# Kernel tuning notes

Measured on AMD Instinct MI355X. Metric: run time of the kernel, lower is better.

Reference implementation:

```python
import jax, jax.numpy as jnp
import numpy as np

EPS = 1e-3  # tfa LayerNormLSTMCell default norm epsilon

def _ln(z, g, b):
    # layernorm over last axis, per gate: z [B,4,U], g/b [4,U]
    mu = jnp.mean(z, axis=-1, keepdims=True)
    var = jnp.mean((z - mu) ** 2, axis=-1, keepdims=True)
    return g * (z - mu) * jax.lax.rsqrt(var + EPS) + b

def setup_inputs() -> dict:
    key = jax.random.key(0)
    ks = jax.random.split(key, 12)
    B, T, D, U, C = 1024, 100, 300, 512, 14
    sc = lambda k, shape, fan: jax.random.normal(k, shape, jnp.float32) * (1.0 / np.sqrt(fan))
    return {
        "x": jax.random.normal(ks[0], (B, T, D), jnp.float32),
        "mask": jax.random.randint(ks[1], (B, T), 0, 2).astype(jnp.int32),
        # layer 0 (input dim D)
        "W0": sc(ks[2], (D, 4 * U), D), "U0": sc(ks[3], (U, 4 * U), U),
        "b0": jnp.zeros((4 * U,), jnp.float32),
        "g0": jnp.ones((4, U), jnp.float32), "be0": jnp.zeros((4, U), jnp.float32),
        # layer 1 (input dim U)
        "W1": sc(ks[4], (U, 4 * U), U), "U1": sc(ks[5], (U, 4 * U), U),
        "b1": jnp.zeros((4 * U,), jnp.float32),
        "g1": jnp.ones((4, U), jnp.float32), "be1": jnp.zeros((4, U), jnp.float32),
        # dense softmax head
        "Wd": sc(ks[6], (U, C), U), "bd": jnp.zeros((C,), jnp.float32),
    }

def reference(x, mask, W0, U0, b0, g0, be0, W1, U1, b1, g1, be1, Wd, bd):
    B, T, D = x.shape
    U = W0.shape[1] // 4
    params = [(W0, U0, b0, g0, be0), (W1, U1, b1, g1, be1)]

    def step(carry, tins):
        hs, cs = carry
        xt, mt = tins                      # xt [B,D_in], mt [B]
        m = (mt > 0)[:, None]
        inp = xt
        new_hs, new_cs = [], []
        for l in range(2):
            W, Uw, b, g, be = params[l]
            z = (inp @ W + hs[l] @ Uw).reshape(B, 4, U)
            z = _ln(z, g, be) + b.reshape(4, U)
            i_g = jax.nn.sigmoid(z[:, 0])
            f_g = jax.nn.sigmoid(z[:, 1])
            c_g = jnp.tanh(z[:, 2])
            o_g = jax.nn.sigmoid(z[:, 3])
            c = f_g * cs[l] + i_g * c_g
            h = o_g * jnp.tanh(c)
            # keras RNN masking: carry state through masked steps
            h = jnp.where(m, h, hs[l])
            c = jnp.where(m, c, cs[l])
            new_hs.append(h); new_cs.append(c)
            inp = h
        return (tuple(new_hs), tuple(new_cs)), None

    z0 = jnp.zeros((B, U), x.dtype)
    carry0 = ((z0, z0), (z0, z0))
    xs = (jnp.swapaxes(x, 0, 1), mask.T)   # time-major [T,B,...]
    (hs, _), _ = jax.lax.scan(step, carry0, xs)
    h_top = hs[-1]                          # [B,U] = last valid output via mask carry
    return jax.nn.softmax(h_top @ Wd + bd, axis=-1)
```

## Files before the change

kernel.cpp:

```cpp
#include <hip/hip_runtime.h>


typedef _Float16 f16;
typedef _Float16 f16x8 __attribute__((ext_vector_type(8)));
typedef _Float16 f16x4 __attribute__((ext_vector_type(4)));
typedef float f32x4 __attribute__((ext_vector_type(4)));

__global__ __launch_bounds__(256) void transpose_f16(
    const float* __restrict__ W, f16* __restrict__ Bt, int K, int N, int Kp,
    int k_off) {
  __shared__ float s[32][33];
  int n0 = blockIdx.x * 32, k0 = blockIdx.y * 32;
  int tid = threadIdx.x, c = tid & 31, r8 = tid >> 5;
  for (int rr = r8; rr < 32; rr += 8) {
    int k = k0 + rr;
    s[rr][c] = (k < K) ? W[(long)k * N + (n0 + c)] : 0.0f;
  }
  __syncthreads();
  for (int rr = r8; rr < 32; rr += 8)
    Bt[(long)(n0 + rr) * Kp + k_off + (k0 + c)] = (f16)s[c][rr];
}

#define MFMAS(AF, BF)                                                                   \
  acc[0][0] = __builtin_amdgcn_mfma_f32_16x16x32_f16(AF[0], BF[0], acc[0][0], 0, 0, 0); \
  acc[0][1] = __builtin_amdgcn_mfma_f32_16x16x32_f16(AF[0], BF[1], acc[0][1], 0, 0, 0); \
  acc[1][0] = __builtin_amdgcn_mfma_f32_16x16x32_f16(AF[1], BF[0], acc[1][0], 0, 0, 0); \
  acc[1][1] = __builtin_amdgcn_mfma_f32_16x16x32_f16(AF[1], BF[1], acc[1][1], 0, 0, 0); \
  acc[2][0] = __builtin_amdgcn_mfma_f32_16x16x32_f16(AF[2], BF[0], acc[2][0], 0, 0, 0); \
  acc[2][1] = __builtin_amdgcn_mfma_f32_16x16x32_f16(AF[2], BF[1], acc[2][1], 0, 0, 0); \
  acc[3][0] = __builtin_amdgcn_mfma_f32_16x16x32_f16(AF[3], BF[0], acc[3][0], 0, 0, 0); \
  acc[3][1] = __builtin_amdgcn_mfma_f32_16x16x32_f16(AF[3], BF[1], acc[3][1], 0, 0, 0);

__global__ __launch_bounds__(256) void gemm_x0(
    const float* __restrict__ x, long lda, const f16* __restrict__ W0t,
    f16* __restrict__ z0x, int full) {
  __shared__ f16 xs[64][340];
  __shared__ f16 st[64][136];
  int tid = threadIdx.x;
  long bm0 = (long)blockIdx.x * 64;

  for (int p = 0; p < 20; ++p) {
    unsigned idx = (unsigned)tid + p * 256u;
    unsigned r = idx / 80u, s = idx - r * 80u;
    f16x4 h4 = {};
    if (s < 75u) {
      f32x4 v = *(const f32x4*)(x + (bm0 + r) * lda + s * 4u);
      h4[0] = (f16)v[0]; h4[1] = (f16)v[1];
      h4[2] = (f16)v[2]; h4[3] = (f16)v[3];
    }
    *(f16x4*)&xs[r][s * 4u] = h4;
  }
  __syncthreads();

  int lane = tid & 63, w = tid >> 6;
  int l15 = lane & 15, quad = lane >> 4;

  for (int nc = 0; nc < 16; ++nc) {
    long bn0 = (long)nc * 128 + w * 32;
    const f16* bw = W0t + (bn0 + l15) * 320L + quad * 8;
    f32x4 acc[4][2] = {};
#pragma unroll
    for (int k0 = 0; k0 < 320; k0 += 32) {
      f16x8 af[4], bf[2];
#pragma unroll
      for (int i = 0; i < 4; ++i)
        af[i] = *(const f16x8*)&xs[l15 + i * 16][quad * 8 + k0];
      bf[0] = *(const f16x8*)(bw + k0);
      bf[1] = *(const f16x8*)(bw + 16 * 320 + k0);
      MFMAS(af, bf)
    }
    __syncthreads();
#pragma unroll
    for (int i = 0; i < 4; ++i)
#pragma unroll
      for (int j = 0; j < 2; ++j)
#pragma unroll
        for (int r = 0; r < 4; ++r)
          st[i * 16 + quad * 4 + r][w * 32 + j * 16 + l15] = (f16)acc[i][j][r];
    __syncthreads();
    {
      int r = tid >> 2, cc = (tid & 3) * 32;
      f16* dst;
      if (full) {
        unsigned rr = (unsigned)(bm0 + r);
        unsigned b = rr / 100u, t = rr - b * 100u;
        dst = z0x + (long)t * 2097152 + (long)b * 2048 + nc * 128 + cc;
      } else {
        dst = z0x + (bm0 + r) * 2048 + nc * 128 + cc;
      }
      const f16x8* s8 = (const f16x8*)&st[r][cc];
      f16x8* d8 = (f16x8*)dst;
      d8[0] = s8[0]; d8[1] = s8[1]; d8[2] = s8[2]; d8[3] = s8[3];
    }
  }
}

#define LD8(AF, BF, A0, B0, LDB, K0)                       \
  AF[0] = *(const f16x8*)((A0) + (K0));                    \
  AF[1] = *(const f16x8*)((A0) + 16 * 1024 + (K0));        \
  AF[2] = *(const f16x8*)((A0) + 32 * 1024 + (K0));        \
  AF[3] = *(const f16x8*)((A0) + 48 * 1024 + (K0));        \
  BF[0] = *(const f16x8*)((B0) + (K0));                    \
  BF[1] = *(const f16x8*)((B0) + 16 * (LDB) + (K0));       \
  BF[2] = *(const f16x8*)((B0) + 32 * (LDB) + (K0));       \
  BF[3] = *(const f16x8*)((B0) + 48 * (LDB) + (K0));

#define MM16(AF, BF)                                                              \
  {                                                                               \
    _Pragma("unroll") for (int i_ = 0; i_ < 4; ++i_)                              \
    _Pragma("unroll") for (int j_ = 0; j_ < 4; ++j_)                              \
      acc[i_][j_] = __builtin_amdgcn_mfma_f32_16x16x32_f16(AF[i_], BF[j_],        \
                                                            acc[i_][j_], 0, 0, 0); \
  }

#define GEMM_PIPE4W(A0, B0, LDB, KTOT)                           \
  {                                                              \
    f16x8 aA[4], bA[4], aB[4], bB[4];                            \
    f16x8 aC[4], bC[4], aD[4], bD[4];                            \
    LD8(aA, bA, A0, B0, LDB, 0)                                  \
    LD8(aB, bB, A0, B0, LDB, 32)                                 \
    LD8(aC, bC, A0, B0, LDB, 64)                                 \
    LD8(aD, bD, A0, B0, LDB, 96)                                 \
    for (int k0 = 0; k0 + 224 < (KTOT); k0 += 128) {             \
      MM16(aA, bA) LD8(aA, bA, A0, B0, LDB, k0 + 128)            \
      MM16(aB, bB) LD8(aB, bB, A0, B0, LDB, k0 + 160)            \
      MM16(aC, bC) LD8(aC, bC, A0, B0, LDB, k0 + 192)            \
      MM16(aD, bD) LD8(aD, bD, A0, B0, LDB, k0 + 224)            \
    }                                                            \
    MM16(aA, bA) MM16(aB, bB) MM16(aC, bC) MM16(aD, bD)          \
  }

__global__ __launch_bounds__(256, 1) void gemm_step(
    const f16* __restrict__ h01, const f16* __restrict__ U0t,
    const f16* __restrict__ WU1t, const f16* __restrict__ cin0,
    float* __restrict__ zA, float* __restrict__ zB, int do0, int do1) {
  int y = blockIdx.y;
  int prob = y >> 3;
  if (prob ? !do1 : !do0) return;
  int tid = threadIdx.x;
  int lane = tid & 63, w = tid >> 6;
  int wr = w >> 1, wc = w & 1;
  int l15 = lane & 15, quad = lane >> 4;
  long bm0 = (long)(y & 7) * 128 + wr * 64;
  long bn0 = (long)blockIdx.x * 128 + wc * 64;
  long arow = (bm0 + l15) * 1024 + quad * 8;

  f32x4 acc[4][4] = {};

  if (prob == 0) {
    const f16* a0 = h01 + arow;
    const f16* b0 = U0t + (bn0 + l15) * 512L + quad * 8;
    GEMM_PIPE4W(a0, b0, 512, 512)
  } else {
    const f16* a0 = h01 + arow;
    const f16* b0 = WU1t + (bn0 + l15) * 1024L + quad * 8;
    GEMM_PIPE4W(a0, b0, 1024, 1024)
  }

  float* Z = prob ? zB : zA;
#pragma unroll
  for (int i = 0; i < 4; ++i) {
    long row = bm0 + i * 16 + quad * 4;
#pragma unroll
    for (int j = 0; j < 4; ++j) {
      long col = bn0 + j * 16 + l15;
#pragma unroll
      for (int r = 0; r < 4; ++r) {
        float v = acc[i][j][r];
        if (prob == 0) v += (float)cin0[(row + r) * 2048 + col];
        Z[(row + r) * 2048 + col] = v;
      }
    }
  }
}

__global__ __launch_bounds__(256) void ln_gates2(
    const float* __restrict__ zA, const float* __restrict__ zB,
    const float* __restrict__ g0, const float* __restrict__ be0,
    const float* __restrict__ bs0, const float* __restrict__ g1,
    const float* __restrict__ be1, const float* __restrict__ bs1,
    const int* __restrict__ mask, int t,
    f16* __restrict__ h01, float* __restrict__ c0, float* __restrict__ c1,
    int do0, int do1) {
  __shared__ float act[2048];
  int layer = blockIdx.x >> 10;
  if (layer ? !do1 : !do0) return;
  int b = blockIdx.x & 1023;
  const float* z = layer ? zB : zA;
  const float* gamma = layer ? g1 : g0;
  const float* beta = layer ? be1 : be0;
  const float* bias = layer ? bs1 : bs0;
  f16* h = h01 + layer * 512;
  float* c = layer ? c1 : c0;
  int tm = layer ? (t - 1) : t;

  int tid = threadIdx.x;
  int w = tid >> 6, lane = tid & 63;

  const float* zb = z + (long)b * 2048 + w * 512;
  f32x4 zv[2];
  float sum = 0.0f, sq = 0.0f;
#pragma unroll
  for (int i = 0; i < 2; ++i) {
    f32x4 v = *(const f32x4*)(zb + lane * 4 + 256 * i);
    zv[i] = v;
#pragma unroll
    for (int e = 0; e < 4; ++e) {
      sum += v[e];
      sq += v[e] * v[e];
    }
  }
#pragma unroll
  for (int off = 32; off; off >>= 1) {
    sum += __shfl_xor(sum, off);
    sq += __shfl_xor(sq, off);
  }
  float mu = sum * (1.0f / 512.0f);
  float var = sq * (1.0f / 512.0f) - mu * mu;
  float is = rsqrtf(var + 1e-3f);

#pragma unroll
  for (int i = 0; i < 2; ++i) {
    int k = w * 512 + lane * 4 + 256 * i;
    f32x4 g = *(const f32x4*)(gamma + k);
    f32x4 be = *(const f32x4*)(beta + k);
    f32x4 bi = *(const f32x4*)(bias + k);
    f32x4 av;
#pragma unroll
    for (int e = 0; e < 4; ++e) {
      float val = g[e] * (zv[i][e] - mu) * is + be[e] + bi[e];
      float a;
      if (w == 2) {
        a = 2.0f / (1.0f + __expf(-2.0f * val)) - 1.0f;
      } else {
        a = 1.0f / (1.0f + __expf(-val));
      }
      av[e] = a;
    }
    *(f32x4*)(act + k) = av;
  }
  __syncthreads();

  bool m = mask[(long)b * 100 + tm] > 0;
#pragma unroll
  for (int i = 0; i < 2; ++i) {
    int u = tid + 256 * i;
    float co = c[(long)b * 512 + u];
    float ho = (float)h[(long)b * 1024 + u];
    float cn = act[512 + u] * co + act[u] * act[1024 + u];
    float th = 2.0f / (1.0f + __expf(-2.0f * cn)) - 1.0f;
    float hn = act[1536 + u] * th;
    h[(long)b * 1024 + u] = (f16)(m ? hn : ho);
    c[(long)b * 512 + u] = m ? cn : co;
  }
}

__global__ __launch_bounds__(64) void head_kernel(
    const f16* __restrict__ h01, const float* __restrict__ Wd,
    const float* __restrict__ bd, float* __restrict__ out) {
  __shared__ float hs[512];
  __shared__ float lg[16];
  int b = blockIdx.x, tid = threadIdx.x;
#pragma unroll
  for (int i = 0; i < 8; ++i)
    hs[tid + 64 * i] = (float)h01[(long)b * 1024 + 512 + tid + 64 * i];
  __syncthreads();
  if (tid < 14) {
    float s = bd[tid];
    for (int k = 0; k < 512; ++k) s += hs[k] * Wd[k * 14 + tid];
    lg[tid] = s;
  }
  __syncthreads();
  if (tid < 14) {
    float mx = lg[0];
#pragma unroll
    for (int i = 1; i < 14; ++i) mx = fmaxf(mx, lg[i]);
    float e = __expf(lg[tid] - mx);
    float den = 0.0f;
#pragma unroll
    for (int i = 0; i < 14; ++i) den += __expf(lg[i] - mx);
    out[(long)b * 14 + tid] = e / den;
  }
}

extern "C" void kernel_launch(void* const* d_in, const int* in_sizes, int n_in,
                              void* d_out, int out_size, void* d_ws, size_t ws_size,
                              hipStream_t stream) {
  const float* x   = (const float*)d_in[0];
  const int* mask  = (const int*)d_in[1];
  const float* W0  = (const float*)d_in[2];
  const float* U0w = (const float*)d_in[3];
  const float* b0  = (const float*)d_in[4];
  const float* g0  = (const float*)d_in[5];
  const float* be0 = (const float*)d_in[6];
  const float* W1  = (const float*)d_in[7];
  const float* U1w = (const float*)d_in[8];
  const float* b1  = (const float*)d_in[9];
  const float* g1  = (const float*)d_in[10];
  const float* be1 = (const float*)d_in[11];
  const float* Wd  = (const float*)d_in[12];
  const float* bd  = (const float*)d_in[13];
  float* out = (float*)d_out;

  char* p = (char*)d_ws;
  const size_t MB = (size_t)1 << 20;
  f16*   h01  = (f16*)(p + 0);
  float* c0   = (float*)(p + 2 * MB);
  float* c1   = (float*)(p + 4 * MB);
  float* zA   = (float*)(p + 6 * MB);
  float* zB   = (float*)(p + 14 * MB);
  f16*   W0t  = (f16*)(p + 22 * MB);
  f16*   U0t  = (f16*)(p + 22 * MB + 1310720);
  f16*   WU1t = (f16*)(p + 22 * MB + 1310720 + 2097152);
  f16*   zX   = (f16*)(p + 30 * MB);
  f16*   z0x  = (f16*)(p + 34 * MB);

  const bool hoist = ws_size >= (size_t)434 * MB;

  hipMemsetAsync(p, 0, 6 * MB, stream);

  transpose_f16<<<dim3(64, 10), 256, 0, stream>>>(W0,  W0t, 300, 2048, 320, 0);
  transpose_f16<<<dim3(64, 16), 256, 0, stream>>>(U0w, U0t, 512, 2048, 512, 0);
  transpose_f16<<<dim3(64, 16), 256, 0, stream>>>(W1,  WU1t, 512, 2048, 1024, 0);
  transpose_f16<<<dim3(64, 16), 256, 0, stream>>>(U1w, WU1t, 512, 2048, 1024, 512);

  if (hoist) {
    gemm_x0<<<1600, 256, 0, stream>>>(x, 300, W0t, z0x, 1);
  }

  for (int t = 0; t <= 100; ++t) {
    int do0 = (t < 100) ? 1 : 0;
    int do1 = (t >= 1) ? 1 : 0;
    const f16* cin0;
    if (hoist) {
      cin0 = z0x + (long)t * 2097152;
    } else {
      if (do0) gemm_x0<<<16, 256, 0, stream>>>(x + (long)t * 300, 30000, W0t, zX, 0);
      cin0 = zX;
    }
    gemm_step<<<dim3(16, 16), 256, 0, stream>>>(
        h01, U0t, WU1t, cin0, zA, zB, do0, do1);
    ln_gates2<<<2048, 256, 0, stream>>>(
        zA, zB, g0, be0, b0, g1, be1, b1, mask, t, h01, c0, c1, do0, do1);
  }

  head_kernel<<<1024, 64, 0, stream>>>(h01, Wd, bd, out);
}
```

Measured before the change: 5.156 ms.

## Fuse input projection into per-step GEMM and halve GEMM tile width

Replaces the hoisted whole-sequence x@W0 precompute, which wrote a large f16 gate buffer, with a conversion of x to padded f16 followed by an in-step x@W0 GEMM fused ahead of the h@U0 product in layer 0. The per-step GEMM tile shrinks from 128 to 64 columns, doubling the grid to 32x16 blocks with launch bounds allowing two blocks per CU, which gives more parallelism and lower register pressure. This removes the large intermediate write and read of precomputed gates. In exchange, layer-0 blocks each step do extra K=320 work and the per-step critical path gets longer.

Result: slower. 5.343 ms (+3.6%).

```diff
diff --git a/kernel.cpp b/kernel.cpp
--- a/kernel.cpp
+++ b/kernel.cpp
@@ -21,118 +21,90 @@
     Bt[(long)(n0 + rr) * Kp + k_off + (k0 + c)] = (f16)s[c][rr];
 }
 
-#define MFMAS(AF, BF)                                                                   \
-  acc[0][0] = __builtin_amdgcn_mfma_f32_16x16x32_f16(AF[0], BF[0], acc[0][0], 0, 0, 0); \
-  acc[0][1] = __builtin_amdgcn_mfma_f32_16x16x32_f16(AF[0], BF[1], acc[0][1], 0, 0, 0); \
-  acc[1][0] = __builtin_amdgcn_mfma_f32_16x16x32_f16(AF[1], BF[0], acc[1][0], 0, 0, 0); \
-  acc[1][1] = __builtin_amdgcn_mfma_f32_16x16x32_f16(AF[1], BF[1], acc[1][1], 0, 0, 0); \
-  acc[2][0] = __builtin_amdgcn_mfma_f32_16x16x32_f16(AF[2], BF[0], acc[2][0], 0, 0, 0); \
-  acc[2][1] = __builtin_amdgcn_mfma_f32_16x16x32_f16(AF[2], BF[1], acc[2][1], 0, 0, 0); \
-  acc[3][0] = __builtin_amdgcn_mfma_f32_16x16x32_f16(AF[3], BF[0], acc[3][0], 0, 0, 0); \
-  acc[3][1] = __builtin_amdgcn_mfma_f32_16x16x32_f16(AF[3], BF[1], acc[3][1], 0, 0, 0);
-
-__global__ __launch_bounds__(256) void gemm_x0(
-    const float* __restrict__ x, long lda, const f16* __restrict__ W0t,
-    f16* __restrict__ z0x, int full) {
-  __shared__ f16 xs[64][340];
-  __shared__ f16 st[64][136];
-  int tid = threadIdx.x;
-  long bm0 = (long)blockIdx.x * 64;
-
-  for (int p = 0; p < 20; ++p) {
-    unsigned idx = (unsigned)tid + p * 256u;
-    unsigned r = idx / 80u, s = idx - r * 80u;
-    f16x4 h4 = {};
-    if (s < 75u) {
-      f32x4 v = *(const f32x4*)(x + (bm0 + r) * lda + s * 4u);
-      h4[0] = (f16)v[0]; h4[1] = (f16)v[1];
-      h4[2] = (f16)v[2]; h4[3] = (f16)v[3];
-    }
-    *(f16x4*)&xs[r][s * 4u] = h4;
-  }
-  __syncthreads();
-
-  int lane = tid & 63, w = tid >> 6;
-  int l15 = lane & 15, quad = lane >> 4;
-
-  for (int nc = 0; nc < 16; ++nc) {
-    long bn0 = (long)nc * 128 + w * 32;
-    const f16* bw = W0t + (bn0 + l15) * 320L + quad * 8;
-    f32x4 acc[4][2] = {};
-#pragma unroll
-    for (int k0 = 0; k0 < 320; k0 += 32) {
-      f16x8 af[4], bf[2];
-#pragma unroll
-      for (int i = 0; i < 4; ++i)
-        af[i] = *(const f16x8*)&xs[l15 + i * 16][quad * 8 + k0];
-      bf[0] = *(const f16x8*)(bw + k0);
-      bf[1] = *(const f16x8*)(bw + 16 * 320 + k0);
-      MFMAS(af, bf)
-    }
-    __syncthreads();
-#pragma unroll
-    for (int i = 0; i < 4; ++i)
-#pragma unroll
-      for (int j = 0; j < 2; ++j)
-#pragma unroll
-        for (int r = 0; r < 4; ++r)
-          st[i * 16 + quad * 4 + r][w * 32 + j * 16 + l15] = (f16)acc[i][j][r];
-    __syncthreads();
-    {
-      int r = tid >> 2, cc = (tid & 3) * 32;
-      f16* dst;
-      if (full) {
-        unsigned rr = (unsigned)(bm0 + r);
-        unsigned b = rr / 100u, t = rr - b * 100u;
-        dst = z0x + (long)t * 2097152 + (long)b * 2048 + nc * 128 + cc;
-      } else {
-        dst = z0x + (bm0 + r) * 2048 + nc * 128 + cc;
-      }
-      const f16x8* s8 = (const f16x8*)&st[r][cc];
-      f16x8* d8 = (f16x8*)dst;
-      d8[0] = s8[0]; d8[1] = s8[1]; d8[2] = s8[2]; d8[3] = s8[3];
-    }
-  }
-}
-
-#define LD8(AF, BF, A0, B0, LDB, K0)                       \
+__global__ __launch_bounds__(256) void convert_x(
+    const float* __restrict__ x, long lda, f16* __restrict__ xh, int rows,
+    int tmode) {
+  int idx = blockIdx.x * 256 + threadIdx.x;
+  if (idx >= rows * 40) return;
+  int r = idx / 40, c8 = (idx - r * 40) * 8;
+  const float* src;
+  if (tmode) {
+    int t = r >> 10, b = r & 1023;
+    src = x + (long)b * 30000 + (long)t * 300;
+  } else {
+    src = x + (long)r * lda;
+  }
+  f16x8 h8;
+  if (c8 + 8 <= 300) {
+    f32x4 lo = *(const f32x4*)(src + c8);
+    f32x4 hi = *(const f32x4*)(src + c8 + 4);
+#pragma unroll
+    for (int e = 0; e < 4; ++e) {
+      h8[e] = (f16)lo[e];
+      h8[4 + e] = (f16)hi[e];
+    }
+  } else {
+#pragma unroll
+    for (int e = 0; e < 8; ++e) {
+      int k = c8 + e;
+      h8[e] = (k < 300) ? (f16)src[k] : (f16)0.f;
+    }
+  }
+  *(f16x8*)(xh + (long)r * 320 + c8) = h8;
+}
+
+#define LD6(AF, BF, A0, LDA, B0, LDB, K0)                  \
   AF[0] = *(const f16x8*)((A0) + (K0));                    \
-  AF[1] = *(const f16x8*)((A0) + 16 * 1024 + (K0));        \
-  AF[2] = *(const f16x8*)((A0) + 32 * 1024 + (K0));        \
-  AF[3] = *(const f16x8*)((A0) + 48 * 1024 + (K0));        \
+  AF[1] = *(const f16x8*)((A0) + 16 * (LDA) + (K0));       \
+  AF[2] = *(const f16x8*)((A0) + 32 * (LDA) + (K0));       \
+  AF[3] = *(const f16x8*)((A0) + 48 * (LDA) + (K0));       \
   BF[0] = *(const f16x8*)((B0) + (K0));                    \
-  BF[1] = *(const f16x8*)((B0) + 16 * (LDB) + (K0));       \
-  BF[2] = *(const f16x8*)((B0) + 32 * (LDB) + (K0));       \
-  BF[3] = *(const f16x8*)((B0) + 48 * (LDB) + (K0));
-
-#define MM16(AF, BF)                                                              \
+  BF[1] = *(const f16x8*)((B0) + 16 * (LDB) + (K0));
+
+#define MM8(AF, BF)                                                               \
   {                                                                               \
     _Pragma("unroll") for (int i_ = 0; i_ < 4; ++i_)                              \
-    _Pragma("unroll") for (int j_ = 0; j_ < 4; ++j_)                              \
+    _Pragma("unroll") for (int j_ = 0; j_ < 2; ++j_)                              \
       acc[i_][j_] = __builtin_amdgcn_mfma_f32_16x16x32_f16(AF[i_], BF[j_],        \
                                                             acc[i_][j_], 0, 0, 0); \
   }
 
-#define GEMM_PIPE4W(A0, B0, LDB, KTOT)                           \
+#define PIPE4(A0, LDA, B0, LDB, KTOT)                            \
   {                                                              \
-    f16x8 aA[4], bA[4], aB[4], bB[4];                            \
-    f16x8 aC[4], bC[4], aD[4], bD[4];                            \
-    LD8(aA, bA, A0, B0, LDB, 0)                                  \
-    LD8(aB, bB, A0, B0, LDB, 32)                                 \
-    LD8(aC, bC, A0, B0, LDB, 64)                                 \
-    LD8(aD, bD, A0, B0, LDB, 96)                                 \
+    f16x8 aA[4], bA[2], aB[4], bB[2];                            \
+    f16x8 aC[4], bC[2], aD[4], bD[2];                            \
+    LD6(aA, bA, A0, LDA, B0, LDB, 0)                             \
+    LD6(aB, bB, A0, LDA, B0, LDB, 32)                            \
+    LD6(aC, bC, A0, LDA, B0, LDB, 64)                            \
+    LD6(aD, bD, A0, LDA, B0, LDB, 96)                            \
     for (int k0 = 0; k0 + 224 < (KTOT); k0 += 128) {             \
-      MM16(aA, bA) LD8(aA, bA, A0, B0, LDB, k0 + 128)            \
-      MM16(aB, bB) LD8(aB, bB, A0, B0, LDB, k0 + 160)            \
-      MM16(aC, bC) LD8(aC, bC, A0, B0, LDB, k0 + 192)            \
-      MM16(aD, bD) LD8(aD, bD, A0, B0, LDB, k0 + 224)            \
+      MM8(aA, bA) LD6(aA, bA, A0, LDA, B0, LDB, k0 + 128)        \
+      MM8(aB, bB) LD6(aB, bB, A0, LDA, B0, LDB, k0 + 160)        \
+      MM8(aC, bC) LD6(aC, bC, A0, LDA, B0, LDB, k0 + 192)        \
+      MM8(aD, bD) LD6(aD, bD, A0, LDA, B0, LDB, k0 + 224)        \
     }                                                            \
-    MM16(aA, bA) MM16(aB, bB) MM16(aC, bC) MM16(aD, bD)          \
-  }
-
-__global__ __launch_bounds__(256, 1) void gemm_step(
-    const f16* __restrict__ h01, const f16* __restrict__ U0t,
-    const f16* __restrict__ WU1t, const f16* __restrict__ cin0,
+    MM8(aA, bA) MM8(aB, bB) MM8(aC, bC) MM8(aD, bD)              \
+  }
+
+#define PIPE2(A0, LDA, B0, LDB, KTOT)                            \
+  {                                                              \
+    f16x8 aE[4], bE[2], aF[4], bF[2];                            \
+    LD6(aE, bE, A0, LDA, B0, LDB, 0)                             \
+    int k0 = 0;                                                  \
+    for (; k0 + 64 < (KTOT); k0 += 64) {                         \
+      LD6(aF, bF, A0, LDA, B0, LDB, k0 + 32)                     \
+      MM8(aE, bE)                                                \
+      LD6(aE, bE, A0, LDA, B0, LDB, k0 + 64)                     \
+      MM8(aF, bF)                                                \
+    }                                                            \
+    LD6(aF, bF, A0, LDA, B0, LDB, k0 + 32)                       \
+    MM8(aE, bE) MM8(aF, bF)                                      \
+  }
+
+__global__ __launch_bounds__(256, 2) void gemm_step(
+    const f16* __restrict__ xh_t, const f16* __restrict__ h01,
+    const f16* __restrict__ W0t, const f16* __restrict__ U0t,
+    const f16* __restrict__ WU1t,
     float* __restrict__ zA, float* __restrict__ zB, int do0, int do1) {
   int y = blockIdx.y;
   int prob = y >> 3;
@@ -142,19 +114,25 @@
   int wr = w >> 1, wc = w & 1;
   int l15 = lane & 15, quad = lane >> 4;
   long bm0 = (long)(y & 7) * 128 + wr * 64;
-  long bn0 = (long)blockIdx.x * 128 + wc * 64;
-  long arow = (bm0 + l15) * 1024 + quad * 8;
-
-  f32x4 acc[4][4] = {};
+  long bn0 = (long)blockIdx.x * 64 + wc * 32;
+
+  f32x4 acc[4][2] = {};
 
   if (prob == 0) {
-    const f16* a0 = h01 + arow;
-    const f16* b0 = U0t + (bn0 + l15) * 512L + quad * 8;
-    GEMM_PIPE4W(a0, b0, 512, 512)
+    {
+      const f16* a0 = xh_t + (bm0 + l15) * 320 + quad * 8;
+      const f16* b0 = W0t + (bn0 + l15) * 320L + quad * 8;
+      PIPE2(a0, 320, b0, 320, 320)
+    }
+    {
+      const f16* a0 = h01 + (bm0 + l15) * 1024 + quad * 8;
+      const f16* b0 = U0t + (bn0 + l15) * 512L + quad * 8;
+      PIPE4(a0, 1024, b0, 512, 512)
+    }
   } else {
-    const f16* a0 = h01 + arow;
+    const f16* a0 = h01 + (bm0 + l15) * 1024 + quad * 8;
     const f16* b0 = WU1t + (bn0 + l15) * 1024L + quad * 8;
-    GEMM_PIPE4W(a0, b0, 1024, 1024)
+    PIPE4(a0, 1024, b0, 1024, 1024)
   }
 
   float* Z = prob ? zB : zA;
@@ -162,14 +140,11 @@
   for (int i = 0; i < 4; ++i) {
     long row = bm0 + i * 16 + quad * 4;
 #pragma unroll
-    for (int j = 0; j < 4; ++j) {
+    for (int j = 0; j < 2; ++j) {
       long col = bn0 + j * 16 + l15;
 #pragma unroll
-      for (int r = 0; r < 4; ++r) {
-        float v = acc[i][j][r];
-        if (prob == 0) v += (float)cin0[(row + r) * 2048 + col];
-        Z[(row + r) * 2048 + col] = v;
-      }
+      for (int r = 0; r < 4; ++r)
+        Z[(row + r) * 2048 + col] = acc[i][j][r];
     }
   }
 }
@@ -312,10 +287,8 @@
   f16*   W0t  = (f16*)(p + 22 * MB);
   f16*   U0t  = (f16*)(p + 22 * MB + 1310720);
   f16*   WU1t = (f16*)(p + 22 * MB + 1310720 + 2097152);
-  f16*   zX   = (f16*)(p + 30 * MB);
-  f16*   z0x  = (f16*)(p + 34 * MB);
-
-  const bool hoist = ws_size >= (size_t)434 * MB;
+  f16*   xh   = (f16*)(p + 30 * MB);
+  const bool fullx = ws_size >= (size_t)93 * MB;
 
   hipMemsetAsync(p, 0, 6 * MB, stream);
 
@@ -324,22 +297,24 @@
   transpose_f16<<<dim3(64, 16), 256, 0, stream>>>(W1,  WU1t, 512, 2048, 1024, 0);
   transpose_f16<<<dim3(64, 16), 256, 0, stream>>>(U1w, WU1t, 512, 2048, 1024, 512);
 
-  if (hoist) {
-    gemm_x0<<<1600, 256, 0, stream>>>(x, 300, W0t, z0x, 1);
+  if (fullx) {
+    convert_x<<<(102400 * 40 + 255) / 256, 256, 0, stream>>>(x, 0, xh, 102400, 1);
   }
 
   for (int t = 0; t <= 100; ++t) {
     int do0 = (t < 100) ? 1 : 0;
     int do1 = (t >= 1) ? 1 : 0;
-    const f16* cin0;
-    if (hoist) {
-      cin0 = z0x + (long)t * 2097152;
+    const f16* xh_t;
+    if (fullx) {
+      xh_t = xh + (long)t * 1024 * 320;
     } else {
-      if (do0) gemm_x0<<<16, 256, 0, stream>>>(x + (long)t * 300, 30000, W0t, zX, 0);
-      cin0 = zX;
-    }
-    gemm_step<<<dim3(16, 16), 256, 0, stream>>>(
-        h01, U0t, WU1t, cin0, zA, zB, do0, do1);
+      if (do0)
+        convert_x<<<(1024 * 40 + 255) / 256, 256, 0, stream>>>(
+            x + (long)t * 300, 30000, (f16*)(p + 30 * MB), 1024, 0);
+      xh_t = (const f16*)(p + 30 * MB);
+    }
+    gemm_step<<<dim3(32, 16), 256, 0, stream>>>(
+        xh_t, h01, W0t, U0t, WU1t, zA, zB, do0, do1);
     ln_gates2<<<2048, 256, 0, stream>>>(
         zA, zB, g0, be0, b0, g1, be1, b1, mask, t, h01, c0, c1, do0, do1);
   }
```
